# Kernel tuning notes

Measured on AMD Instinct MI355X. Metric: run time of the kernel, lower is better.

The kernel has to match this reference:

```python
import jax, jax.numpy as jnp
import numpy as np

E = 4096      # num hyperedges (events)
H1 = 512      # hidden1
H2 = 128      # hidden2 (latent)
NA, NK, NV = 8192, 4096, 1024   # nodes per type: author / keyword / venue
NNZ = 131072  # nonzeros per incidence matrix
SCALE = 0.02  # weight init scale (keeps tanh/exp in sane range)


def setup_inputs() -> dict:
    key = jax.random.key(0)
    ks = iter(jax.random.split(key, 64))
    nrm = lambda shape, s=SCALE: jax.random.normal(next(ks), shape, jnp.float32) * s
    inp = {}
    for t, N in (("a", NA), ("k", NK), ("v", NV)):
        inp["rows_" + t] = jax.random.randint(next(ks), (NNZ,), 0, N, dtype=jnp.int32)
        inp["cols_" + t] = jax.random.randint(next(ks), (NNZ,), 0, E, dtype=jnp.int32)
        inp["vals_" + t] = jax.random.uniform(next(ks), (NNZ,), jnp.float32)
        inp["Wn_" + t] = nrm((E, H1));  inp["bn_" + t] = jnp.zeros((H1,), jnp.float32)
        inp["Wzm_" + t] = nrm((H1, H2)); inp["bzm_" + t] = jnp.zeros((H2,), jnp.float32)
        inp["Wzs_" + t] = nrm((H1, H2)); inp["bzs_" + t] = jnp.zeros((H2,), jnp.float32)
        inp["We_" + t] = nrm((N, H1));  inp["be_" + t] = jnp.zeros((H1,), jnp.float32)
        inp["eps_" + t] = jax.random.normal(next(ks), (N, H2), jnp.float32)
    inp["Watt"] = nrm((H1, H1 // 2)); inp["batt"] = jnp.zeros((H1 // 2,), jnp.float32)
    inp["uatt"] = nrm((H1 // 2,), 0.1)
    inp["Wem"] = nrm((H1, H2)); inp["bem"] = jnp.zeros((H2,), jnp.float32)
    inp["Wes"] = nrm((H1, H2)); inp["bes"] = jnp.zeros((H2,), jnp.float32)
    inp["eps_e"] = jax.random.normal(next(ks), (E, H2), jnp.float32)
    return inp


def _type_branch(rows, cols, vals, N, Wn, bn, Wzm, bzm, Wzs, bzs, We, be, eps):
    # node encoder: tanh(sparse_inc @ Wn + bn);  sparse_inc is [N, E] in COO form
    h = jnp.tanh(jax.ops.segment_sum(vals[:, None] * Wn[cols], rows, num_segments=N) + bn)
    zm = h @ Wzm + bzm
    zs = h @ Wzs + bzs
    z = zm + eps * jnp.exp(zs)          # reparameterization
    # edge encoder: tanh(sparse_inc^T @ We + be) -> [E, H1]
    e = jnp.tanh(jax.ops.segment_sum(vals[:, None] * We[rows], cols, num_segments=E) + be)
    return zm, z, e


def _forward(rows_a, cols_a, vals_a, Wn_a, bn_a, Wzm_a, bzm_a, Wzs_a, bzs_a, We_a, be_a, eps_a,
             rows_k, cols_k, vals_k, Wn_k, bn_k, Wzm_k, bzm_k, Wzs_k, bzs_k, We_k, be_k, eps_k,
             rows_v, cols_v, vals_v, Wn_v, bn_v, Wzm_v, bzm_v, Wzs_v, bzs_v, We_v, be_v, eps_v,
             Watt, batt, uatt, Wem, bem, Wes, bes, eps_e):
    zm_a, z_a, e_a = _type_branch(rows_a, cols_a, vals_a, NA, Wn_a, bn_a, Wzm_a, bzm_a, Wzs_a, bzs_a, We_a, be_a, eps_a)
    zm_k, z_k, e_k = _type_branch(rows_k, cols_k, vals_k, NK, Wn_k, bn_k, Wzm_k, bzm_k, Wzs_k, bzs_k, We_k, be_k, eps_k)
    zm_v, z_v, e_v = _type_branch(rows_v, cols_v, vals_v, NV, Wn_v, bn_v, Wzm_v, bzm_v, Wzs_v, bzs_v, We_v, be_v, eps_v)

    # HyperedgeAttention over node types: [E, T=3, H1]
    edge_embeds = jnp.stack([e_a, e_k, e_v], axis=1)
    u = jnp.tanh(jnp.einsum('eth,hd->etd', edge_embeds, Watt) + batt)
    scores = jnp.einsum('etd,d->et', u, uatt)
    alphas = jax.nn.softmax(scores, axis=1)                  # [E, T]
    edge_embed = jnp.einsum('et,eth->eh', alphas, edge_embeds)  # [E, H1]

    zem = edge_embed @ Wem + bem
    zes = edge_embed @ Wes + bes
    ze = zem + eps_e * jnp.exp(zes)

    # InnerDecoder: z_node @ z_edge^T per type, flattened (sampled and mean variants)
    recon = jnp.concatenate([
        (z_a @ ze.T).ravel(), (z_k @ ze.T).ravel(), (z_v @ ze.T).ravel(),
        (zm_a @ zem.T).ravel(), (zm_k @ zem.T).ravel(), (zm_v @ zem.T).ravel(),
    ])
    return recon


def reference(rows_a, cols_a, vals_a, rows_k, cols_k, vals_k, rows_v, cols_v, vals_v,
              Wn_a, bn_a, Wzm_a, bzm_a, Wzs_a, bzs_a, We_a, be_a, eps_a,
              Wn_k, bn_k, Wzm_k, bzm_k, Wzs_k, bzs_k, We_k, be_k, eps_k,
              Wn_v, bn_v, Wzm_v, bzm_v, Wzs_v, bzs_v, We_v, be_v, eps_v,
              Watt, batt, uatt, Wem, bem, Wes, bes, eps_e):
    return _forward(rows_a, cols_a, vals_a, Wn_a, bn_a, Wzm_a, bzm_a, Wzs_a, bzs_a, We_a, be_a, eps_a,
                    rows_k, cols_k, vals_k, Wn_k, bn_k, Wzm_k, bzm_k, Wzs_k, bzs_k, We_k, be_k, eps_k,
                    rows_v, cols_v, vals_v, Wn_v, bn_v, Wzm_v, bzm_v, Wzs_v, bzs_v, We_v, be_v, eps_v,
                    Watt, batt, uatt, Wem, bem, Wes, bes, eps_e)
```

## Files before the change

### kernel.cpp

```cpp
#include <hip/hip_runtime.h>
#include <hip/hip_bf16.h>

#define NE   4096
#define D1   512
#define D2   128
#define NNZV 131072
#define MTOT 13312

typedef __attribute__((ext_vector_type(8))) short bf16x8;
typedef __attribute__((ext_vector_type(4))) float f32x4;

struct Params {
  const int*   rows[3]; const int* cols[3]; const float* vals[3];
  const float* Wn[3];  const float* bn[3];
  const float* Wzm[3]; const float* bzm[3];
  const float* Wzs[3]; const float* bzs[3];
  const float* We[3];  const float* be[3];
  const float* eps[3];
  const float* Watt; const float* batt; const float* uatt;
  const float* Wem;  const float* bem;  const float* Wes; const float* bes;
  const float* eps_e;
  int* cnt[6]; int* ptr[6]; int* cur[6]; int2* spair[6];
  __hip_bfloat16* Wbf[6];
  float* h[3]; float* e[3];
  float* scores;
  __hip_bfloat16* Zbf; __hip_bfloat16* Zmbf; __hip_bfloat16* zebf; __hip_bfloat16* zembf;
  float* out;
  int rowbase[3];
  int n8pre[7];
  int ndw;
};

__device__ __forceinline__ float bf2f(short s) {
  return __uint_as_float((unsigned)(unsigned short)s << 16);
}

__device__ __forceinline__ int nseg_of(int sub) {
  if (sub & 1) return NE;
  int t = sub >> 1;
  return t == 0 ? 8192 : (t == 1 ? 4096 : 1024);
}

__global__ void prep_kernel(Params p) {
  int i = blockIdx.x * blockDim.x + threadIdx.x;
  if (i < p.ndw) { ((int*)p.cnt[0])[i] = 0; return; }
  int c = i - p.ndw;
  if (c >= p.n8pre[6]) return;
  int s = 0;
#pragma unroll
  for (int k = 1; k < 6; ++k) if (c >= p.n8pre[k]) s = k;
  int off8 = c - p.n8pre[s];
  int t = s >> 1;
  const float* src = (s & 1) ? p.We[t] : p.Wn[t];
  __hip_bfloat16* dst = p.Wbf[s];
  const float4 a = *(const float4*)&src[(size_t)off8 * 8];
  const float4 b = *(const float4*)&src[(size_t)off8 * 8 + 4];
  bf16x8 o;
  o[0] = (short)__bfloat16_as_ushort(__float2bfloat16(a.x));
  o[1] = (short)__bfloat16_as_ushort(__float2bfloat16(a.y));
  o[2] = (short)__bfloat16_as_ushort(__float2bfloat16(a.z));
  o[3] = (short)__bfloat16_as_ushort(__float2bfloat16(a.w));
  o[4] = (short)__bfloat16_as_ushort(__float2bfloat16(b.x));
  o[5] = (short)__bfloat16_as_ushort(__float2bfloat16(b.y));
  o[6] = (short)__bfloat16_as_ushort(__float2bfloat16(b.z));
  o[7] = (short)__bfloat16_as_ushort(__float2bfloat16(b.w));
  *(bf16x8*)&dst[(size_t)off8 * 8] = o;
}

__global__ void hist_kernel(Params p) {
  int i = blockIdx.x * blockDim.x + threadIdx.x;
  if (i >= 6 * NNZV) return;
  int sub = i >> 17, idx = i & (NNZV - 1);
  int type = sub >> 1, dir = sub & 1;
  int seg = dir ? p.cols[type][idx] : p.rows[type][idx];
  atomicAdd(&p.cnt[sub][seg], 1);
}

__global__ __launch_bounds__(1024) void scan_kernel(Params p) {
  int sub = blockIdx.x;
  int n = nseg_of(sub);
  const int* cnt = p.cnt[sub];
  int* ptr = p.ptr[sub];
  int* cur = p.cur[sub];
  __shared__ int lds[1024];
  int tid = threadIdx.x;
  int per = (n + 1023) >> 10;
  int base = tid * per;
  int s = 0;
  for (int q = 0; q < per; ++q) { int ix = base + q; if (ix < n) s += cnt[ix]; }
  lds[tid] = s;
  __syncthreads();
  for (int off = 1; off < 1024; off <<= 1) {
    int v = (tid >= off) ? lds[tid - off] : 0;
    __syncthreads();
    lds[tid] += v;
    __syncthreads();
  }
  int prefix = (tid == 0) ? 0 : lds[tid - 1];
  for (int q = 0; q < per; ++q) {
    int ix = base + q;
    if (ix < n) { int c = cnt[ix]; ptr[ix] = prefix; cur[ix] = prefix; prefix += c; }
  }
  if (tid == 1023) ptr[n] = lds[1023];
}

__global__ void scatter_kernel(Params p) {
  int i = blockIdx.x * blockDim.x + threadIdx.x;
  if (i >= 6 * NNZV) return;
  int sub = i >> 17, idx = i & (NNZV - 1);
  int type = sub >> 1, dir = sub & 1;
  int seg = dir ? p.cols[type][idx] : p.rows[type][idx];
  int oth = dir ? p.rows[type][idx] : p.cols[type][idx];
  int pos = atomicAdd(&p.cur[sub][seg], 1);
  p.spair[sub][pos] = make_int2(oth, __float_as_int(p.vals[type][idx]));
}

__global__ __launch_bounds__(128) void spmm_kernel(Params p) {
  int g = blockIdx.x * 2 + (threadIdx.x >> 6);
  int sub, seg;
  if      (g <  8192) { sub = 0; seg = g;         }
  else if (g < 12288) { sub = 1; seg = g - 8192;  }
  else if (g < 16384) { sub = 2; seg = g - 12288; }
  else if (g < 20480) { sub = 3; seg = g - 16384; }
  else if (g < 21504) { sub = 4; seg = g - 20480; }
  else                { sub = 5; seg = g - 21504; }
  int type = sub >> 1, dir = sub & 1;
  const __hip_bfloat16* W = p.Wbf[sub];
  const float* bias = dir ? p.be[type] : p.bn[type];
  float* outp       = dir ? p.e[type]  : p.h[type];
  const int*  ptr  = p.ptr[sub];
  const int2* pair = p.spair[sub];
  int lane = threadIdx.x & 63;
  int c0 = lane * 8;
  float acc[8];
#pragma unroll
  for (int j = 0; j < 8; ++j) acc[j] = 0.f;
  int q0 = ptr[seg], q1 = ptr[seg + 1];
  int q = q0;
  for (; q + 4 <= q1; q += 4) {
    int2 pr0 = pair[q], pr1 = pair[q + 1], pr2 = pair[q + 2], pr3 = pair[q + 3];
    const bf16x8 w0 = *(const bf16x8*)(W + (size_t)pr0.x * D1 + c0);
    const bf16x8 w1 = *(const bf16x8*)(W + (size_t)pr1.x * D1 + c0);
    const bf16x8 w2 = *(const bf16x8*)(W + (size_t)pr2.x * D1 + c0);
    const bf16x8 w3 = *(const bf16x8*)(W + (size_t)pr3.x * D1 + c0);
    float v0 = __int_as_float(pr0.y), v1 = __int_as_float(pr1.y);
    float v2 = __int_as_float(pr2.y), v3 = __int_as_float(pr3.y);
#pragma unroll
    for (int j = 0; j < 8; ++j)
      acc[j] += v0 * bf2f(w0[j]) + v1 * bf2f(w1[j]) + v2 * bf2f(w2[j]) + v3 * bf2f(w3[j]);
  }
  for (; q < q1; ++q) {
    int2 pr = pair[q];
    const bf16x8 wv = *(const bf16x8*)(W + (size_t)pr.x * D1 + c0);
    float v = __int_as_float(pr.y);
#pragma unroll
    for (int j = 0; j < 8; ++j) acc[j] += v * bf2f(wv[j]);
  }
  const float4 b0 = *(const float4*)&bias[c0];
  const float4 b1 = *(const float4*)&bias[c0 + 4];
  float4 o0, o1;
  o0.x = tanhf(acc[0] + b0.x); o0.y = tanhf(acc[1] + b0.y);
  o0.z = tanhf(acc[2] + b0.z); o0.w = tanhf(acc[3] + b0.w);
  o1.x = tanhf(acc[4] + b1.x); o1.y = tanhf(acc[5] + b1.y);
  o1.z = tanhf(acc[6] + b1.z); o1.w = tanhf(acc[7] + b1.w);
  *(float4*)&outp[(size_t)seg * D1 + c0]     = o0;
  *(float4*)&outp[(size_t)seg * D1 + c0 + 4] = o1;
}

__global__ __launch_bounds__(256) void zmzs_kernel(Params p) {
  __shared__ __align__(16) float hs[32 * D1];
  int b = blockIdx.x;
  int type, blk;
  if      (b < 256) { type = 0; blk = b;       }
  else if (b < 384) { type = 1; blk = b - 256; }
  else              { type = 2; blk = b - 384; }
  int row0 = blk * 32;
  const float* hsrc = p.h[type] + (size_t)row0 * D1;
  for (int i4 = threadIdx.x; i4 < 32 * (D1 / 4); i4 += 256)
    ((float4*)hs)[i4] = ((const float4*)hsrc)[i4];
  __syncthreads();
  int jp = threadIdx.x & 63, rg = threadIdx.x >> 6;
  int j = jp * 2;
  const float* Wm = p.Wzm[type];
  const float* Ws = p.Wzs[type];
  float am[8][2], as[8][2];
#pragma unroll
  for (int r = 0; r < 8; ++r) { am[r][0]=am[r][1]=as[r][0]=as[r][1]=0.f; }
  for (int hh = 0; hh < D1; hh += 4) {
    float2 wm[4], ws[4];
#pragma unroll
    for (int q = 0; q < 4; ++q) {
      wm[q] = *(const float2*)&Wm[(size_t)(hh + q) * D2 + j];
      ws[q] = *(const float2*)&Ws[(size_t)(hh + q) * D2 + j];
    }
#pragma unroll
    for (int r = 0; r < 8; ++r) {
      const float4 ev = *(const float4*)&hs[(rg * 8 + r) * D1 + hh];
      am[r][0] += ev.x*wm[0].x + ev.y*wm[1].x + ev.z*wm[2].x + ev.w*wm[3].x;
      am[r][1] += ev.x*wm[0].y + ev.y*wm[1].y + ev.z*wm[2].y + ev.w*wm[3].y;
      as[r][0] += ev.x*ws[0].x + ev.y*ws[1].x + ev.z*ws[2].x + ev.w*ws[3].x;
      as[r][1] += ev.x*ws[0].y + ev.y*ws[1].y + ev.z*ws[2].y + ev.w*ws[3].y;
    }
  }
  int base = p.rowbase[type];
  const float* eps = p.eps[type];
  float bm0 = p.bzm[type][j], bm1 = p.bzm[type][j+1];
  float bs0 = p.bzs[type][j], bs1 = p.bzs[type][j+1];
#pragma unroll
  for (int r = 0; r < 8; ++r) {
    int row = row0 + rg * 8 + r;
    float zm0 = am[r][0] + bm0, zm1 = am[r][1] + bm1;
    float zs0 = as[r][0] + bs0, zs1 = as[r][1] + bs1;
    float e0v = eps[(size_t)row * D2 + j], e1v = eps[(size_t)row * D2 + j + 1];
    float z0 = zm0 + e0v * expf(zs0), z1 = zm1 + e1v * expf(zs1);
    size_t oi = (size_t)(base + row) * D2 + j;
    p.Zmbf[oi]   = __float2bfloat16(zm0); p.Zmbf[oi+1] = __float2bfloat16(zm1);
    p.Zbf[oi]    = __float2bfloat16(z0);  p.Zbf[oi+1]  = __float2bfloat16(z1);
  }
}

__global__ __launch_bounds__(256) void scorecomb_kernel(Params p) {
  __shared__ __align__(16) float em[24 * D1];
  __shared__ float sc[24];
  __shared__ float alpha[8][3];
  int e0 = blockIdx.x * 8;
  int tid = threadIdx.x;
  for (int i4 = tid; i4 < 24 * (D1 / 4); i4 += 256) {
    int r = i4 >> 7, h4 = i4 & 127;
    int el = r / 3, t = r - el * 3;
    ((float4*)em)[i4] = ((const float4*)(p.e[t] + (size_t)(e0 + el) * D1))[h4];
  }
  __syncthreads();
  int lane = tid & 63, w = tid >> 6;
  {
    int d0 = lane * 4;
    float acc[6][4];
#pragma unroll
    for (int r = 0; r < 6; ++r) { acc[r][0]=acc[r][1]=acc[r][2]=acc[r][3]=0.f; }
    for (int hh = 0; hh < D1; hh += 4) {
      float4 w0 = *(const float4*)&p.Watt[(size_t)(hh+0) * 256 + d0];
      float4 w1 = *(const float4*)&p.Watt[(size_t)(hh+1) * 256 + d0];
      float4 w2 = *(const float4*)&p.Watt[(size_t)(hh+2) * 256 + d0];
      float4 w3 = *(const float4*)&p.Watt[(size_t)(hh+3) * 256 + d0];
#pragma unroll
      for (int r = 0; r < 6; ++r) {
        const float4 ev = *(const float4*)&em[(w * 6 + r) * D1 + hh];
        acc[r][0] += ev.x*w0.x + ev.y*w1.x + ev.z*w2.x + ev.w*w3.x;
        acc[r][1] += ev.x*w0.y + ev.y*w1.y + ev.z*w2.y + ev.w*w3.y;
        acc[r][2] += ev.x*w0.z + ev.y*w1.z + ev.z*w2.z + ev.w*w3.z;
        acc[r][3] += ev.x*w0.w + ev.y*w1.w + ev.z*w2.w + ev.w*w3.w;
      }
    }
    const float4 u4 = *(const float4*)&p.uatt[d0];
    const float4 b4 = *(const float4*)&p.batt[d0];
#pragma unroll
    for (int r = 0; r < 6; ++r) {
      float s = u4.x * tanhf(acc[r][0] + b4.x) + u4.y * tanhf(acc[r][1] + b4.y)
              + u4.z * tanhf(acc[r][2] + b4.z) + u4.w * tanhf(acc[r][3] + b4.w);
#pragma unroll
      for (int off = 32; off > 0; off >>= 1) s += __shfl_down(s, off, 64);
      if (lane == 0) sc[w * 6 + r] = s;
    }
  }
  __syncthreads();
  if (tid < 8) {
    float s0 = sc[tid * 3 + 0], s1 = sc[tid * 3 + 1], s2 = sc[tid * 3 + 2];
    float m = fmaxf(s0, fmaxf(s1, s2));
    float a0 = expf(s0 - m), a1 = expf(s1 - m), a2 = expf(s2 - m);
    float inv = 1.f / (a0 + a1 + a2);
    alpha[tid][0] = a0 * inv; alpha[tid][1] = a1 * inv; alpha[tid][2] = a2 * inv;
  }
  __syncthreads();
  float4 ve[4];
#pragma unroll
  for (int k = 0; k < 4; ++k) {
    int i4 = tid + k * 256;
    int el = i4 >> 7, h4 = i4 & 127;
    float4 va = ((const float4*)em)[(el * 3 + 0) * 128 + h4];
    float4 vk = ((const float4*)em)[(el * 3 + 1) * 128 + h4];
    float4 vv = ((const float4*)em)[(el * 3 + 2) * 128 + h4];
    float a0 = alpha[el][0], a1 = alpha[el][1], a2 = alpha[el][2];
    ve[k].x = a0*va.x + a1*vk.x + a2*vv.x;
    ve[k].y = a0*va.y + a1*vk.y + a2*vv.y;
    ve[k].z = a0*va.z + a1*vk.z + a2*vv.z;
    ve[k].w = a0*va.w + a1*vk.w + a2*vv.w;
  }
  __syncthreads();
#pragma unroll
  for (int k = 0; k < 4; ++k)
    ((float4*)em)[tid + k * 256] = ve[k];
  __syncthreads();
  int jp = tid & 63, eg = tid >> 6;
  int j = jp * 2;
  float am[2][2], as[2][2];
#pragma unroll
  for (int r = 0; r < 2; ++r) { am[r][0]=am[r][1]=as[r][0]=as[r][1]=0.f; }
  for (int hh = 0; hh < D1; hh += 4) {
    float2 wm[4], ws[4];
#pragma unroll
    for (int q = 0; q < 4; ++q) {
      wm[q] = *(const float2*)&p.Wem[(size_t)(hh + q) * D2 + j];
      ws[q] = *(const float2*)&p.Wes[(size_t)(hh + q) * D2 + j];
    }
#pragma unroll
    for (int r = 0; r < 2; ++r) {
      const float4 ev = *(const float4*)&em[(eg * 2 + r) * D1 + hh];
      am[r][0] += ev.x*wm[0].x + ev.y*wm[1].x + ev.z*wm[2].x + ev.w*wm[3].x;
      am[r][1] += ev.x*wm[0].y + ev.y*wm[1].y + ev.z*wm[2].y + ev.w*wm[3].y;
      as[r][0] += ev.x*ws[0].x + ev.y*ws[1].x + ev.z*ws[2].x + ev.w*ws[3].x;
      as[r][1] += ev.x*ws[0].y + ev.y*ws[1].y + ev.z*ws[2].y + ev.w*ws[3].y;
    }
  }
  float bm0 = p.bem[j], bm1 = p.bem[j+1], bs0 = p.bes[j], bs1 = p.bes[j+1];
#pragma unroll
  for (int r = 0; r < 2; ++r) {
    int e = e0 + eg * 2 + r;
    float zm0 = am[r][0] + bm0, zm1 = am[r][1] + bm1;
    float zs0 = as[r][0] + bs0, zs1 = as[r][1] + bs1;
    float e0v = p.eps_e[(size_t)e * D2 + j], e1v = p.eps_e[(size_t)e * D2 + j + 1];
    float z0 = zm0 + e0v * expf(zs0), z1 = zm1 + e1v * expf(zs1);
    size_t oi = (size_t)e * D2 + j;
    p.zembf[oi]   = __float2bfloat16(zm0); p.zembf[oi+1] = __float2bfloat16(zm1);
    p.zebf[oi]    = __float2bfloat16(z0);  p.zebf[oi+1]  = __float2bfloat16(z1);
  }
}

#define DT_N 128
__global__ __launch_bounds__(256) void decode_kernel(Params p) {
  __shared__ __align__(16) float cs[64][DT_N + 4];
  int which = blockIdx.z;
  const __hip_bfloat16* A = which ? p.Zmbf  : p.Zbf;
  const __hip_bfloat16* B = which ? p.zembf : p.zebf;
  float* C = p.out + (size_t)which * MTOT * NE;
  int n0 = blockIdx.x * DT_N;
  int m0 = blockIdx.y * 64;
  int wid  = threadIdx.x >> 6;
  int lane = threadIdx.x & 63;
  int rloc = lane & 15;
  int kg   = lane >> 4;
  int mrow = m0 + wid * 16 + rloc;
  bf16x8 a[4];
#pragma unroll
  for (int kk = 0; kk < 4; ++kk)
    a[kk] = *(const bf16x8*)(A + (size_t)mrow * D2 + kk * 32 + kg * 8);
  f32x4 acc[DT_N / 16];
  f32x4 zero = {0.f, 0.f, 0.f, 0.f};
#pragma unroll
  for (int nf = 0; nf < DT_N / 16; ++nf) acc[nf] = zero;
#pragma unroll
  for (int nf = 0; nf < DT_N / 16; ++nf) {
    int ncol = n0 + nf * 16 + rloc;
#pragma unroll
    for (int kk = 0; kk < 4; ++kk) {
      bf16x8 bv = *(const bf16x8*)(B + (size_t)ncol * D2 + kk * 32 + kg * 8);
      acc[nf] = __builtin_amdgcn_mfma_f32_16x16x32_bf16(a[kk], bv, acc[nf], 0, 0, 0);
    }
  }
#pragma unroll
  for (int nf = 0; nf < DT_N / 16; ++nf)
#pragma unroll
    for (int jj = 0; jj < 4; ++jj)
      cs[wid * 16 + kg * 4 + jj][nf * 16 + rloc] = acc[nf][jj];
  __syncthreads();
  int r_l  = threadIdx.x >> 5;
  int c4   = (threadIdx.x & 31) * 4;
#pragma unroll
  for (int it = 0; it < 8; ++it) {
    int r = it * 8 + r_l;
    f32x4 v = *(const f32x4*)&cs[r][c4];
    __builtin_nontemporal_store(v, (f32x4*)&C[(size_t)(m0 + r) * NE + n0 + c4]);
  }
}

extern "C" void kernel_launch(void* const* d_in, const int* in_sizes, int n_in,
                              void* d_out, int out_size, void* d_ws, size_t ws_size,
                              hipStream_t stream) {
  (void)in_sizes; (void)n_in; (void)out_size; (void)ws_size;
  static const int Ns[3] = {8192, 4096, 1024};
  static const int NsegH[6] = {8192, 4096, 4096, 4096, 1024, 4096};

  Params p;
  for (int t = 0; t < 3; ++t) {
    const int o = t * 12;
    p.rows[t] = (const int*)d_in[o + 0];
    p.cols[t] = (const int*)d_in[o + 1];
    p.vals[t] = (const float*)d_in[o + 2];
    p.Wn[t]   = (const float*)d_in[o + 3];
    p.bn[t]   = (const float*)d_in[o + 4];
    p.Wzm[t]  = (const float*)d_in[o + 5];
    p.bzm[t]  = (const float*)d_in[o + 6];
    p.Wzs[t]  = (const float*)d_in[o + 7];
    p.bzs[t]  = (const float*)d_in[o + 8];
    p.We[t]   = (const float*)d_in[o + 9];
    p.be[t]   = (const float*)d_in[o + 10];
    p.eps[t]  = (const float*)d_in[o + 11];
  }
  p.Watt  = (const float*)d_in[36];
  p.batt  = (const float*)d_in[37];
  p.uatt  = (const float*)d_in[38];
  p.Wem   = (const float*)d_in[39];
  p.bem   = (const float*)d_in[40];
  p.Wes   = (const float*)d_in[41];
  p.bes   = (const float*)d_in[42];
  p.eps_e = (const float*)d_in[43];
  p.out = (float*)d_out;
  p.rowbase[0] = 0; p.rowbase[1] = 8192; p.rowbase[2] = 12288;

  char* ws = (char*)d_ws;
  size_t off = 0;
  auto alloc = [&](size_t bytes) -> char* {
    char* r = ws + off;
    off += (bytes + 255) & ~(size_t)255;
    return r;
  };
  for (int s = 0; s < 6; ++s) p.cnt[s] = (int*)alloc((size_t)(NsegH[s] + 1) * 4);
  size_t cnt_bytes = off;
  for (int s = 0; s < 6; ++s) {
    p.ptr[s]   = (int*)alloc((size_t)(NsegH[s] + 1) * 4);
    p.cur[s]   = (int*)alloc((size_t)(NsegH[s] + 1) * 4);
    p.spair[s] = (int2*)alloc((size_t)NNZV * 8);
  }
  for (int s = 0; s < 6; ++s) {
    int t = s >> 1;
    int nrows = (s & 1) ? Ns[t] : NE;
    p.Wbf[s] = (__hip_bfloat16*)alloc((size_t)nrows * D1 * 2);
  }
  for (int t = 0; t < 3; ++t) p.h[t] = (float*)alloc((size_t)Ns[t] * D1 * 4);
  for (int t = 0; t < 3; ++t) p.e[t] = (float*)alloc((size_t)NE * D1 * 4);
  p.scores = (float*)alloc((size_t)NE * 3 * 4);
  p.Zbf    = (__hip_bfloat16*)alloc((size_t)MTOT * D2 * 2);
  p.Zmbf   = (__hip_bfloat16*)alloc((size_t)MTOT * D2 * 2);
  p.zebf   = (__hip_bfloat16*)alloc((size_t)NE * D2 * 2);
  p.zembf  = (__hip_bfloat16*)alloc((size_t)NE * D2 * 2);

  p.ndw = (int)(cnt_bytes >> 2);
  p.n8pre[0] = 0;
  for (int s = 0; s < 6; ++s) {
    int t = s >> 1;
    int nrows = (s & 1) ? Ns[t] : NE;
    p.n8pre[s + 1] = p.n8pre[s] + nrows * (D1 / 8);
  }

  int prep_threads = p.ndw + p.n8pre[6];
  prep_kernel     <<<(prep_threads + 255) / 256, 256, 0, stream>>>(p);
  hist_kernel     <<<(6 * NNZV + 255) / 256, 256, 0, stream>>>(p);
  scan_kernel     <<<6, 1024, 0, stream>>>(p);
  scatter_kernel  <<<(6 * NNZV + 255) / 256, 256, 0, stream>>>(p);
  spmm_kernel     <<<12800, 128, 0, stream>>>(p);
  zmzs_kernel     <<<416, 256, 0, stream>>>(p);
  scorecomb_kernel<<<512, 256, 0, stream>>>(p);
  decode_kernel   <<<dim3(NE / DT_N, 208, 2), 256, 0, stream>>>(p);
}
```

Baseline: 638.6 us.

## Compute zm/zs projections with bf16 MFMA and store node hidden states in bf16

The node-encoder SpMM now writes its tanh output as bf16 instead of fp32, and the zm/zs projection kernel is rewritten from an LDS-tiled fp32 FMA loop into a bf16 MFMA 16x16x32 kernel. The prep kernel gains a step that converts the Wzm/Wzs weights to bf16 and transposes them so B fragments load contiguously. This targets the FMA-bound projection and halves the h write/read traffic, at the cost of bf16 rounding of h and the weights, plus uncoalesced scattered writes in the transpose.

```diff
diff --git a/kernel.cpp b/kernel.cpp
--- a/kernel.cpp
+++ b/kernel.cpp
@@ -22,8 +22,10 @@
   const float* eps_e;
   int* cnt[6]; int* ptr[6]; int* cur[6]; int2* spair[6];
   __hip_bfloat16* Wbf[6];
-  float* h[3]; float* e[3];
-  float* scores;
+  __hip_bfloat16* hbf[3];
+  __hip_bfloat16* Wzmt[3];
+  __hip_bfloat16* Wzst[3];
+  float* e[3];
   __hip_bfloat16* Zbf; __hip_bfloat16* Zmbf; __hip_bfloat16* zebf; __hip_bfloat16* zembf;
   float* out;
   int rowbase[3];
@@ -45,26 +47,37 @@
   int i = blockIdx.x * blockDim.x + threadIdx.x;
   if (i < p.ndw) { ((int*)p.cnt[0])[i] = 0; return; }
   int c = i - p.ndw;
-  if (c >= p.n8pre[6]) return;
-  int s = 0;
-#pragma unroll
-  for (int k = 1; k < 6; ++k) if (c >= p.n8pre[k]) s = k;
-  int off8 = c - p.n8pre[s];
-  int t = s >> 1;
-  const float* src = (s & 1) ? p.We[t] : p.Wn[t];
-  __hip_bfloat16* dst = p.Wbf[s];
-  const float4 a = *(const float4*)&src[(size_t)off8 * 8];
-  const float4 b = *(const float4*)&src[(size_t)off8 * 8 + 4];
-  bf16x8 o;
-  o[0] = (short)__bfloat16_as_ushort(__float2bfloat16(a.x));
-  o[1] = (short)__bfloat16_as_ushort(__float2bfloat16(a.y));
-  o[2] = (short)__bfloat16_as_ushort(__float2bfloat16(a.z));
-  o[3] = (short)__bfloat16_as_ushort(__float2bfloat16(a.w));
-  o[4] = (short)__bfloat16_as_ushort(__float2bfloat16(b.x));
-  o[5] = (short)__bfloat16_as_ushort(__float2bfloat16(b.y));
-  o[6] = (short)__bfloat16_as_ushort(__float2bfloat16(b.z));
-  o[7] = (short)__bfloat16_as_ushort(__float2bfloat16(b.w));
-  *(bf16x8*)&dst[(size_t)off8 * 8] = o;
+  if (c < p.n8pre[6]) {
+    int s = 0;
+#pragma unroll
+    for (int k = 1; k < 6; ++k) if (c >= p.n8pre[k]) s = k;
+    int off8 = c - p.n8pre[s];
+    int t = s >> 1;
+    const float* src = (s & 1) ? p.We[t] : p.Wn[t];
+    __hip_bfloat16* dst = p.Wbf[s];
+    const float4 a = *(const float4*)&src[(size_t)off8 * 8];
+    const float4 b = *(const float4*)&src[(size_t)off8 * 8 + 4];
+    bf16x8 o;
+    o[0] = (short)__bfloat16_as_ushort(__float2bfloat16(a.x));
+    o[1] = (short)__bfloat16_as_ushort(__float2bfloat16(a.y));
+    o[2] = (short)__bfloat16_as_ushort(__float2bfloat16(a.z));
+    o[3] = (short)__bfloat16_as_ushort(__float2bfloat16(a.w));
+    o[4] = (short)__bfloat16_as_ushort(__float2bfloat16(b.x));
+    o[5] = (short)__bfloat16_as_ushort(__float2bfloat16(b.y));
+    o[6] = (short)__bfloat16_as_ushort(__float2bfloat16(b.z));
+    o[7] = (short)__bfloat16_as_ushort(__float2bfloat16(b.w));
+    *(bf16x8*)&dst[(size_t)off8 * 8] = o;
+    return;
+  }
+  int c2 = c - p.n8pre[6];
+  if (c2 >= 6 * D1 * D2) return;
+  int m = c2 >> 16;
+  int e = c2 & 65535;
+  int t = m >> 1;
+  const float* src = (m & 1) ? p.Wzs[t] : p.Wzm[t];
+  __hip_bfloat16* dst = (m & 1) ? p.Wzst[t] : p.Wzmt[t];
+  int k = e >> 7, n = e & 127;
+  dst[n * D1 + k] = __float2bfloat16(src[e]);
 }
 
 __global__ void hist_kernel(Params p) {
@@ -127,7 +140,6 @@
   int type = sub >> 1, dir = sub & 1;
   const __hip_bfloat16* W = p.Wbf[sub];
   const float* bias = dir ? p.be[type] : p.bn[type];
-  float* outp       = dir ? p.e[type]  : p.h[type];
   const int*  ptr  = p.ptr[sub];
   const int2* pair = p.spair[sub];
   int lane = threadIdx.x & 63;
@@ -158,64 +170,72 @@
   }
   const float4 b0 = *(const float4*)&bias[c0];
   const float4 b1 = *(const float4*)&bias[c0 + 4];
-  float4 o0, o1;
-  o0.x = tanhf(acc[0] + b0.x); o0.y = tanhf(acc[1] + b0.y);
-  o0.z = tanhf(acc[2] + b0.z); o0.w = tanhf(acc[3] + b0.w);
-  o1.x = tanhf(acc[4] + b1.x); o1.y = tanhf(acc[5] + b1.y);
-  o1.z = tanhf(acc[6] + b1.z); o1.w = tanhf(acc[7] + b1.w);
-  *(float4*)&outp[(size_t)seg * D1 + c0]     = o0;
-  *(float4*)&outp[(size_t)seg * D1 + c0 + 4] = o1;
-}
-
-__global__ __launch_bounds__(256) void zmzs_kernel(Params p) {
-  __shared__ __align__(16) float hs[32 * D1];
+  float r[8];
+  r[0] = tanhf(acc[0] + b0.x); r[1] = tanhf(acc[1] + b0.y);
+  r[2] = tanhf(acc[2] + b0.z); r[3] = tanhf(acc[3] + b0.w);
+  r[4] = tanhf(acc[4] + b1.x); r[5] = tanhf(acc[5] + b1.y);
+  r[6] = tanhf(acc[6] + b1.z); r[7] = tanhf(acc[7] + b1.w);
+  if (dir) {
+    float4 o0 = {r[0], r[1], r[2], r[3]};
+    float4 o1 = {r[4], r[5], r[6], r[7]};
+    *(float4*)&p.e[type][(size_t)seg * D1 + c0]     = o0;
+    *(float4*)&p.e[type][(size_t)seg * D1 + c0 + 4] = o1;
+  } else {
+    bf16x8 ob;
+#pragma unroll
+    for (int j = 0; j < 8; ++j) ob[j] = (short)__bfloat16_as_ushort(__float2bfloat16(r[j]));
+    *(bf16x8*)&p.hbf[type][(size_t)seg * D1 + c0] = ob;
+  }
+}
+
+__global__ __launch_bounds__(128) void zmzs_kernel(Params p) {
   int b = blockIdx.x;
   int type, blk;
   if      (b < 256) { type = 0; blk = b;       }
   else if (b < 384) { type = 1; blk = b - 256; }
   else              { type = 2; blk = b - 384; }
   int row0 = blk * 32;
-  const float* hsrc = p.h[type] + (size_t)row0 * D1;
-  for (int i4 = threadIdx.x; i4 < 32 * (D1 / 4); i4 += 256)
-    ((float4*)hs)[i4] = ((const float4*)hsrc)[i4];
-  __syncthreads();
-  int jp = threadIdx.x & 63, rg = threadIdx.x >> 6;
-  int j = jp * 2;
-  const float* Wm = p.Wzm[type];
-  const float* Ws = p.Wzs[type];
-  float am[8][2], as[8][2];
-#pragma unroll
-  for (int r = 0; r < 8; ++r) { am[r][0]=am[r][1]=as[r][0]=as[r][1]=0.f; }
-  for (int hh = 0; hh < D1; hh += 4) {
-    float2 wm[4], ws[4];
-#pragma unroll
-    for (int q = 0; q < 4; ++q) {
-      wm[q] = *(const float2*)&Wm[(size_t)(hh + q) * D2 + j];
-      ws[q] = *(const float2*)&Ws[(size_t)(hh + q) * D2 + j];
-    }
-#pragma unroll
-    for (int r = 0; r < 8; ++r) {
-      const float4 ev = *(const float4*)&hs[(rg * 8 + r) * D1 + hh];
-      am[r][0] += ev.x*wm[0].x + ev.y*wm[1].x + ev.z*wm[2].x + ev.w*wm[3].x;
-      am[r][1] += ev.x*wm[0].y + ev.y*wm[1].y + ev.z*wm[2].y + ev.w*wm[3].y;
-      as[r][0] += ev.x*ws[0].x + ev.y*ws[1].x + ev.z*ws[2].x + ev.w*ws[3].x;
-      as[r][1] += ev.x*ws[0].y + ev.y*ws[1].y + ev.z*ws[2].y + ev.w*ws[3].y;
+  const __hip_bfloat16* A  = p.hbf[type];
+  const __hip_bfloat16* Bm = p.Wzmt[type];
+  const __hip_bfloat16* Bs = p.Wzst[type];
+  int wid = threadIdx.x >> 6, lane = threadIdx.x & 63;
+  int rloc = lane & 15, kg = lane >> 4;
+  int mrow = row0 + wid * 16 + rloc;
+  f32x4 accm[8], accs[8];
+  f32x4 zero = {0.f, 0.f, 0.f, 0.f};
+#pragma unroll
+  for (int nf = 0; nf < 8; ++nf) { accm[nf] = zero; accs[nf] = zero; }
+  for (int kk = 0; kk < 16; ++kk) {
+    bf16x8 a = *(const bf16x8*)(A + (size_t)mrow * D1 + kk * 32 + kg * 8);
+#pragma unroll
+    for (int nf = 0; nf < 8; ++nf) {
+      int ncol = nf * 16 + rloc;
+      bf16x8 bm = *(const bf16x8*)(Bm + (size_t)ncol * D1 + kk * 32 + kg * 8);
+      accm[nf] = __builtin_amdgcn_mfma_f32_16x16x32_bf16(a, bm, accm[nf], 0, 0, 0);
+      bf16x8 bs = *(const bf16x8*)(Bs + (size_t)ncol * D1 + kk * 32 + kg * 8);
+      accs[nf] = __builtin_amdgcn_mfma_f32_16x16x32_bf16(a, bs, accs[nf], 0, 0, 0);
     }
   }
   int base = p.rowbase[type];
   const float* eps = p.eps[type];
-  float bm0 = p.bzm[type][j], bm1 = p.bzm[type][j+1];
-  float bs0 = p.bzs[type][j], bs1 = p.bzs[type][j+1];
-#pragma unroll
-  for (int r = 0; r < 8; ++r) {
-    int row = row0 + rg * 8 + r;
-    float zm0 = am[r][0] + bm0, zm1 = am[r][1] + bm1;
-    float zs0 = as[r][0] + bs0, zs1 = as[r][1] + bs1;
-    float e0v = eps[(size_t)row * D2 + j], e1v = eps[(size_t)row * D2 + j + 1];
-    float z0 = zm0 + e0v * expf(zs0), z1 = zm1 + e1v * expf(zs1);
-    size_t oi = (size_t)(base + row) * D2 + j;
-    p.Zmbf[oi]   = __float2bfloat16(zm0); p.Zmbf[oi+1] = __float2bfloat16(zm1);
-    p.Zbf[oi]    = __float2bfloat16(z0);  p.Zbf[oi+1]  = __float2bfloat16(z1);
+  const float* bzm = p.bzm[type];
+  const float* bzs = p.bzs[type];
+  int rbase = row0 + wid * 16 + kg * 4;
+#pragma unroll
+  for (int nf = 0; nf < 8; ++nf) {
+    int col = nf * 16 + rloc;
+    float bm = bzm[col], bs = bzs[col];
+#pragma unroll
+    for (int jj = 0; jj < 4; ++jj) {
+      int row = rbase + jj;
+      float zm = accm[nf][jj] + bm;
+      float zs = accs[nf][jj] + bs;
+      float ep = eps[(size_t)row * D2 + col];
+      float z  = zm + ep * expf(zs);
+      size_t oi = (size_t)(base + row) * D2 + col;
+      p.Zmbf[oi] = __float2bfloat16(zm);
+      p.Zbf[oi]  = __float2bfloat16(z);
+    }
   }
 }
 
@@ -425,9 +445,10 @@
     int nrows = (s & 1) ? Ns[t] : NE;
     p.Wbf[s] = (__hip_bfloat16*)alloc((size_t)nrows * D1 * 2);
   }
-  for (int t = 0; t < 3; ++t) p.h[t] = (float*)alloc((size_t)Ns[t] * D1 * 4);
+  for (int t = 0; t < 3; ++t) p.hbf[t]  = (__hip_bfloat16*)alloc((size_t)Ns[t] * D1 * 2);
+  for (int t = 0; t < 3; ++t) p.Wzmt[t] = (__hip_bfloat16*)alloc((size_t)D2 * D1 * 2);
+  for (int t = 0; t < 3; ++t) p.Wzst[t] = (__hip_bfloat16*)alloc((size_t)D2 * D1 * 2);
   for (int t = 0; t < 3; ++t) p.e[t] = (float*)alloc((size_t)NE * D1 * 4);
-  p.scores = (float*)alloc((size_t)NE * 3 * 4);
   p.Zbf    = (__hip_bfloat16*)alloc((size_t)MTOT * D2 * 2);
   p.Zmbf   = (__hip_bfloat16*)alloc((size_t)MTOT * D2 * 2);
   p.zebf   = (__hip_bfloat16*)alloc((size_t)NE * D2 * 2);
@@ -441,13 +462,13 @@
     p.n8pre[s + 1] = p.n8pre[s] + nrows * (D1 / 8);
   }
 
-  int prep_threads = p.ndw + p.n8pre[6];
+  int prep_threads = p.ndw + p.n8pre[6] + 6 * D1 * D2;
   prep_kernel     <<<(prep_threads + 255) / 256, 256, 0, stream>>>(p);
   hist_kernel     <<<(6 * NNZV + 255) / 256, 256, 0, stream>>>(p);
   scan_kernel     <<<6, 1024, 0, stream>>>(p);
   scatter_kernel  <<<(6 * NNZV + 255) / 256, 256, 0, stream>>>(p);
   spmm_kernel     <<<12800, 128, 0, stream>>>(p);
-  zmzs_kernel     <<<416, 256, 0, stream>>>(p);
+  zmzs_kernel     <<<416, 128, 0, stream>>>(p);
   scorecomb_kernel<<<512, 256, 0, stream>>>(p);
   decode_kernel   <<<dim3(NE / DT_N, 208, 2), 256, 0, stream>>>(p);
 }
```

Measured after the change: 607.4 us. -4.9%, faster.
